# Kernel tuning notes

Hardware: AMD Instinct MI355X
Metric: run time of the kernel (lower is better)

Reference implementation:

```python
import jax, jax.numpy as jnp
import numpy as np
from jax import lax

B, N, C = 2, 4096, 8
MAX_DET = 100
SCORE_THR = 0.01
NMS_THR = 0.5
NEG = -1e30  # sentinel for masked scores


def setup_inputs() -> dict:
    key = jax.random.key(0)
    k1, k2, k3, k4, k5 = jax.random.split(key, 5)
    # valid xyxy boxes: centers in [0,512), extents in [2,66)
    ctr = jax.random.uniform(k1, (B, N, 2), dtype=jnp.float32) * 512.0
    wh = jax.random.uniform(k2, (B, N, 2), dtype=jnp.float32) * 64.0 + 2.0
    boxes = jnp.concatenate([ctr - wh / 2, ctr + wh / 2], axis=-1)  # [B,N,4]
    classification = jax.random.uniform(k3, (B, N, C), dtype=jnp.float32)
    rotation = jax.random.normal(k4, (B, N, 3), dtype=jnp.float32)
    translation = jax.random.normal(k5, (B, N, 3), dtype=jnp.float32)
    return {"boxes": boxes, "classification": classification,
            "rotation": rotation, "translation": translation}


def _pairwise_iou(b):
    # b: [N,4] xyxy, torchvision convention (no +1)
    x1, y1, x2, y2 = b[:, 0], b[:, 1], b[:, 2], b[:, 3]
    area = (x2 - x1) * (y2 - y1)
    ix1 = jnp.maximum(x1[:, None], x1[None, :])
    iy1 = jnp.maximum(y1[:, None], y1[None, :])
    ix2 = jnp.minimum(x2[:, None], x2[None, :])
    iy2 = jnp.minimum(y2[:, None], y2[None, :])
    inter = jnp.clip(ix2 - ix1, 0.0) * jnp.clip(iy2 - iy1, 0.0)
    union = area[:, None] + area[None, :] - inter
    return inter / jnp.maximum(union, 1e-9)


def _nms_keep(boxes, scores, valid):
    # greedy NMS matching torchvision.ops.nms on the `valid` subset.
    order = jnp.argsort(-jnp.where(valid, scores, NEG))  # score-descending
    iou = _pairwise_iou(boxes[order])  # [N,N]
    idx = jnp.arange(N)
    keep0 = valid[order]

    def body(i, keep):
        sup = keep[i] & (iou[i] > NMS_THR) & (idx > i)
        return keep & ~sup

    keep_sorted = lax.fori_loop(0, N, body, keep0)
    return jnp.zeros(N, bool).at[order].set(keep_sorted)


def _filter_image(boxes, cls, rot, trans):
    # boxes [N,4], cls [N,C], rot [N,3], trans [N,3]
    def per_class(scores):
        valid = scores > SCORE_THR
        keep = _nms_keep(boxes, scores, valid)
        return jnp.where(keep, scores, NEG)

    masked = jax.vmap(per_class, in_axes=1)(cls)  # [C,N]
    topv, topi = lax.top_k(masked.reshape(-1), MAX_DET)
    labels = topi // N
    anchors = topi % N
    ok = topv > NEG / 2
    okc = ok[:, None]
    boxes_o = jnp.where(okc, boxes[anchors], -1.0)
    scores_o = jnp.where(ok, topv, -1.0)
    labels_o = jnp.where(ok, labels, -1)
    rot_o = jnp.where(okc, rot[anchors], -1.0)
    trans_o = jnp.where(okc, trans[anchors], -1.0)
    return boxes_o, scores_o, labels_o, rot_o, trans_o


def reference(boxes, classification, rotation, translation):
    return jax.vmap(_filter_image)(boxes, classification, rotation, translation)
```

## Files before the change

kernel.cpp:

```cpp
#include <hip/hip_runtime.h>
#include <hip/hip_bf16.h>
#include <stdint.h>

#define B_ 2
#define N_ 4096
#define C_ 8
#define MAXDET 100
#define SCORE_THR 0.01f
#define NMS_THR 0.5f
#define NEGV -1e30f

typedef unsigned long long u64;

__device__ __forceinline__ unsigned mono_key(float f) {
    unsigned u = __float_as_uint(f);
    return (u & 0x80000000u) ? ~u : (u | 0x80000000u);
}
__device__ __forceinline__ float mono_dec(unsigned m) {
    return (m & 0x80000000u) ? __uint_as_float(m ^ 0x80000000u)
                             : __uint_as_float(~m);
}
__device__ __forceinline__ bool iou_gt_half(float inter, float uni) {
    return (inter + inter - uni) > uni * 0x1p-25f;
}
__device__ __forceinline__ void wave_fence() {
    asm volatile("s_waitcnt lgkmcnt(0)" ::: "memory");
}

__device__ __forceinline__ void ce_shfl(u64 &e0, u64 &e1, int tid, int size,
                                        int stride, bool desc) {
    const int m = stride >> 1;
    bool d = (((2 * tid) & size) == 0) ? desc : !desc;
    bool lower = (tid & m) == 0;
    u64 p0 = __shfl_xor(e0, m, 64);
    u64 p1 = __shfl_xor(e1, m, 64);
    bool takeMax = (d == lower);
    e0 = takeMax ? (e0 > p0 ? e0 : p0) : (e0 < p0 ? e0 : p0);
    e1 = takeMax ? (e1 > p1 ? e1 : p1) : (e1 < p1 ? e1 : p1);
}
__device__ __forceinline__ void ce_intra(u64 &e0, u64 &e1, int tid, int size,
                                         bool desc) {
    bool d = (((2 * tid) & size) == 0) ? desc : !desc;
    if ((e0 < e1) == d) { u64 t = e0; e0 = e1; e1 = t; }
}

__global__ __launch_bounds__(512) void sortA_kernel(
    const float* __restrict__ cls,
    u64* __restrict__ keys)
{
    __shared__ u64 k[1024];
    const int q = blockIdx.x;
    const int bc = blockIdx.y;
    const int b = bc >> 3, c = bc & 7;
    const int tid = threadIdx.x;
    const bool desc = ((q & 1) == 0);

    u64 e0, e1;
    {
        int i0 = q * 1024 + 2 * tid;
        float s0 = cls[((size_t)b * N_ + i0) * C_ + c];
        float s1 = cls[((size_t)b * N_ + i0 + 1) * C_ + c];
        float f0 = (s0 > SCORE_THR) ? s0 : NEGV;
        float f1 = (s1 > SCORE_THR) ? s1 : NEGV;
        e0 = ((u64)mono_key(f0) << 32) | (unsigned)(~i0);
        e1 = ((u64)mono_key(f1) << 32) | (unsigned)(~(i0 + 1));
    }

    #pragma unroll
    for (int size = 2; size <= 128; size <<= 1) {
        #pragma unroll
        for (int stride = size >> 1; stride >= 2; stride >>= 1)
            ce_shfl(e0, e1, tid, size, stride, desc);
        ce_intra(e0, e1, tid, size, desc);
    }
    #pragma unroll
    for (int size = 256; size <= 1024; size <<= 1) {
        k[2 * tid] = e0; k[2 * tid + 1] = e1;
        __syncthreads();
        for (int stride = size >> 1; stride >= 128; stride >>= 1) {
            int pos = 2 * tid - (tid & (stride - 1));
            int par = pos + stride;
            bool d = ((pos & size) == 0) ? desc : !desc;
            u64 a = k[pos], bb = k[par];
            if ((a < bb) == d) { k[pos] = bb; k[par] = a; }
            __syncthreads();
        }
        e0 = k[2 * tid]; e1 = k[2 * tid + 1];
        #pragma unroll
        for (int stride = 64; stride >= 2; stride >>= 1)
            ce_shfl(e0, e1, tid, size, stride, desc);
        ce_intra(e0, e1, tid, size, desc);
    }

    ulonglong2 v; v.x = e0; v.y = e1;
    *(ulonglong2*)&keys[(size_t)bc * N_ + q * 1024 + 2 * tid] = v;
}

__global__ __launch_bounds__(512) void fused_kernel(
    const u64* __restrict__ keys,
    const float* __restrict__ boxes,
    u64* __restrict__ cand)
{
    __shared__ u64 m[4096];
    __shared__ float4 sb192[192];
    __shared__ float  sa192[192];
    __shared__ u64 cm[576];
    __shared__ float4 sbx[64];
    __shared__ u64 shJ[64];
    __shared__ int s_fin;

    const int bc = blockIdx.x;
    const int b = bc >> 3, cls = bc & 7;
    const int tid = threadIdx.x;
    const int lane = tid & 63;
    const int wave = tid >> 6;
    const size_t kbase = (size_t)bc * N_;
    const float4* boxes4 = (const float4*)boxes;

    u64 e0, e1;
    {
        int i = 2 * tid;
        int qq = i >> 8;
        int off = qq * 1024 + ((qq & 1) ? 768 : 0) + (i & 255);
        ulonglong2 v = *(const ulonglong2*)&keys[kbase + off];
        e0 = v.x; e1 = v.y;
    }

    #pragma unroll
    for (int size = 512; size <= 1024; size <<= 1) {
        m[2 * tid] = e0; m[2 * tid + 1] = e1;
        __syncthreads();
        for (int stride = size >> 1; stride >= 128; stride >>= 1) {
            int pos = 2 * tid - (tid & (stride - 1));
            int par = pos + stride;
            bool d = ((pos & size) == 0);
            u64 a = m[pos], bb = m[par];
            if ((a < bb) == d) { m[pos] = bb; m[par] = a; }
            __syncthreads();
        }
        e0 = m[2 * tid]; e1 = m[2 * tid + 1];
        #pragma unroll
        for (int stride = 64; stride >= 2; stride >>= 1)
            ce_shfl(e0, e1, tid, size, stride, true);
        ce_intra(e0, e1, tid, size, true);
    }
    m[2 * tid] = e0; m[2 * tid + 1] = e1;
    __syncthreads();

    if (tid < 192) {
        int orig = (int)(~(unsigned)m[tid]);
        float4 bx = boxes4[(size_t)b * N_ + orig];
        sb192[tid] = bx;
        sa192[tid] = (bx.z - bx.x) * (bx.w - bx.y);
    }
    __syncthreads();

    for (int qq = tid; qq < 576; qq += 512) {
        int r = qq / 3, w = qq - 3 * r;
        int chunk = r >> 6;
        u64 bits = 0ull;
        if (w >= chunk) {
            float4 bi = sb192[r];
            float aarea = sa192[r];
            #pragma unroll 8
            for (int t = 0; t < 64; t++) {
                float4 bj = sb192[w * 64 + t];
                float barea = sa192[w * 64 + t];
                float ix1 = fmaxf(bi.x, bj.x);
                float iy1 = fmaxf(bi.y, bj.y);
                float ix2 = fminf(bi.z, bj.z);
                float iy2 = fminf(bi.w, bj.w);
                float inter = fmaxf(ix2 - ix1, 0.0f) * fmaxf(iy2 - iy1, 0.0f);
                float uni = fmaxf(aarea + barea - inter, 1e-9f);
                if (iou_gt_half(inter, uni)) bits |= (1ull << t);
            }
            if (w == chunk) bits &= ~((2ull << (r & 63)) - 1ull);
        }
        cm[qq] = bits;
    }
    __syncthreads();

    if (wave == 0) {
        u64 remv = 0ull;
        int cc = 0;
        bool fin = false;
        for (int c = 0; c < 3; c++) {
            int p = c * 64 + lane;
            u64 key = m[p];
            float sc = mono_dec((unsigned)(key >> 32));
            u64 validb = __ballot(sc > -1e29f);
            if (validb == 0ull) { fin = true; break; }

            u64 curw = __shfl(remv, c, 64);
            u64 kept = 0ull;
            for (int t = 0; t < 64; t++) {
                u64 iv = cm[(c * 64 + t) * 3 + c];
                u64 bit = 1ull << t;
                if (!(curw & bit) && (validb & bit)) { kept |= bit; curw |= iv; }
            }

            if ((kept >> lane) & 1ull) {
                int rank = cc + __popcll(kept & ((1ull << lane) - 1ull));
                if (rank < 128) {
                    int orig = (int)(~(unsigned)key);
                    unsigned flat = (unsigned)(cls * N_ + orig);
                    cand[bc * 128 + rank] =
                        ((u64)mono_key(sc) << 32) | (unsigned)(~flat);
                }
            }
            cc += __popcll(kept);
            if (cc >= 128) { fin = true; break; }

            if (lane < 3) {
                u64 acc = 0ull;
                for (int t = 0; t < 64; t++)
                    if ((kept >> t) & 1ull) acc |= cm[(c * 64 + t) * 3 + lane];
                remv |= acc;
            }
        }
        if (fin) {
            int filled = cc < 128 ? cc : 128;
            for (int s = lane; s < 128; s += 64)
                if (s >= filled) cand[bc * 128 + s] = 0ull;
        }
        if (lane == 0) s_fin = fin ? 1 : 0;
    }
    __syncthreads();
    if (s_fin) return;

    for (int i = tid; i < 4096; i += 512) m[i] = keys[kbase + i];
    __syncthreads();
    for (int size = 2048; size <= 4096; size <<= 1) {
        for (int stride = size >> 1; stride > 0; stride >>= 1) {
            for (int t = tid; t < 2048; t += 512) {
                int pos = 2 * t - (t & (stride - 1));
                int par = pos + stride;
                bool d = ((pos & size) == 0);
                u64 a = m[pos], bb = m[par];
                if ((a < bb) == d) { m[pos] = bb; m[par] = a; }
            }
            __syncthreads();
        }
    }
    if (wave != 0) return;

    {
        u64 remv = 0ull;
        int cc = 0;
        for (int c = 0; c < 64; c++) {
            int p = c * 64 + lane;
            u64 key = m[p];
            float sc = mono_dec((unsigned)(key >> 32));
            u64 validb = __ballot(sc > -1e29f);
            if (validb == 0ull) break;

            int orig = (int)(~(unsigned)key);
            float4 bl = boxes4[(size_t)b * N_ + orig];
            sbx[lane] = bl;
            wave_fence();
            float al = (bl.z - bl.x) * (bl.w - bl.y);

            u64 intra = 0ull;
            for (int t = 0; t < 64; t++) {
                float4 bj = sbx[t];
                float ab = (bj.z - bj.x) * (bj.w - bj.y);
                float ix1 = fmaxf(bl.x, bj.x);
                float iy1 = fmaxf(bl.y, bj.y);
                float ix2 = fminf(bl.z, bj.z);
                float iy2 = fminf(bl.w, bj.w);
                float inter = fmaxf(ix2 - ix1, 0.0f) * fmaxf(iy2 - iy1, 0.0f);
                float uni = fmaxf(al + ab - inter, 1e-9f);
                if (t > lane && iou_gt_half(inter, uni)) intra |= (1ull << t);
            }
            shJ[lane] = intra;
            wave_fence();

            u64 curw = __shfl(remv, c, 64);
            u64 kept = 0ull;
            for (int t = 0; t < 64; t++) {
                u64 iv = shJ[t];
                u64 bit = 1ull << t;
                if (!(curw & bit) && (validb & bit)) { kept |= bit; curw |= iv; }
            }

            if ((kept >> lane) & 1ull) {
                int rank = cc + __popcll(kept & ((1ull << lane) - 1ull));
                if (rank < 128) {
                    unsigned flat = (unsigned)(cls * N_ + orig);
                    cand[bc * 128 + rank] =
                        ((u64)mono_key(sc) << 32) | (unsigned)(~flat);
                }
            }
            cc += __popcll(kept);
            if (cc >= 128) break;

            if (lane > c) {
                u64 accw = 0ull;
                for (int u = 0; u < 64; u++) {
                    int pj = lane * 64 + u;
                    int oj = (int)(~(unsigned)m[pj]);
                    float4 bj = boxes4[(size_t)b * N_ + oj];
                    float ab = (bj.z - bj.x) * (bj.w - bj.y);
                    bool sup = false;
                    for (int tt = 0; tt < 64; tt++) {
                        if (!((kept >> tt) & 1ull)) continue;
                        float4 br = sbx[tt];
                        float ar = (br.z - br.x) * (br.w - br.y);
                        float ix1 = fmaxf(br.x, bj.x);
                        float iy1 = fmaxf(br.y, bj.y);
                        float ix2 = fminf(br.z, bj.z);
                        float iy2 = fminf(br.w, bj.w);
                        float inter = fmaxf(ix2 - ix1, 0.0f) * fmaxf(iy2 - iy1, 0.0f);
                        float uni = fmaxf(ar + ab - inter, 1e-9f);
                        if (iou_gt_half(inter, uni)) { sup = true; break; }
                    }
                    if (sup) accw |= (1ull << u);
                }
                remv |= accw;
            }
            wave_fence();
        }
        int filled = cc < 128 ? cc : 128;
        for (int s = lane; s < 128; s += 64)
            if (s >= filled) cand[bc * 128 + s] = 0ull;
    }
}

__global__ __launch_bounds__(1024) void merge_kernel(
    const u64* __restrict__ cand,
    const float* __restrict__ boxes,
    const float* __restrict__ rot,
    const float* __restrict__ trans,
    float* __restrict__ out)
{
    __shared__ u64 sk[1024];
    const int b = blockIdx.x;
    const int tid = threadIdx.x;
    const int c = tid >> 7, s = tid & 127;

    int src = (c & 1) ? (c * 128 + (127 - s)) : tid;
    sk[tid] = cand[(size_t)b * 1024 + src];

    for (int size = 256; size <= 1024; size <<= 1) {
        for (int stride = size >> 1; stride > 0; stride >>= 1) {
            __syncthreads();
            int partner = tid ^ stride;
            if (partner > tid) {
                bool desc = ((tid & size) == 0);
                u64 a = sk[tid], bb = sk[partner];
                if ((a < bb) == desc) { sk[tid] = bb; sk[partner] = a; }
            }
        }
    }
    __syncthreads();

    if (tid < MAXDET) {
        u64 key = sk[tid];
        float score = mono_dec((unsigned)(key >> 32));
        bool ok = score > (NEGV * 0.5f);
        unsigned flat = (~(unsigned)key) & 32767u;
        int cc = flat >> 12;
        int n = flat & (N_ - 1);

        float* obox = out;
        float* oscr = out + 800;
        float* olab = out + 1000;
        float* orot = out + 1200;
        float* otrn = out + 1800;

        #pragma unroll
        for (int d = 0; d < 4; d++)
            obox[b * 400 + tid * 4 + d] =
                ok ? boxes[((size_t)b * N_ + n) * 4 + d] : -1.0f;
        oscr[b * MAXDET + tid] = ok ? score : -1.0f;
        olab[b * MAXDET + tid] = ok ? (float)cc : -1.0f;
        #pragma unroll
        for (int d = 0; d < 3; d++) {
            orot[b * 300 + tid * 3 + d] =
                ok ? rot[((size_t)b * N_ + n) * 3 + d] : -1.0f;
            otrn[b * 300 + tid * 3 + d] =
                ok ? trans[((size_t)b * N_ + n) * 3 + d] : -1.0f;
        }
    }
}

extern "C" void kernel_launch(void* const* d_in, const int* in_sizes, int n_in,
                              void* d_out, int out_size, void* d_ws, size_t ws_size,
                              hipStream_t stream) {
    const float* boxes = (const float*)d_in[0];
    const float* cls   = (const float*)d_in[1];
    const float* rot   = (const float*)d_in[2];
    const float* trans = (const float*)d_in[3];
    float* out = (float*)d_out;

    char* w = (char*)d_ws;
    u64* keys = (u64*)w;   w += (size_t)B_ * C_ * N_ * sizeof(u64);
    u64* cand = (u64*)w;   w += (size_t)B_ * C_ * 128 * sizeof(u64);

    sortA_kernel<<<dim3(4, B_ * C_), 512, 0, stream>>>(cls, keys);
    fused_kernel<<<B_ * C_, 512, 0, stream>>>(keys, boxes, cand);
    merge_kernel<<<B_, 1024, 0, stream>>>(cand, boxes, rot, trans, out);
}
```

Before: 97.27 us.

## Fuse sort, NMS and merge into one kernel with last-block election

Replaces the three-kernel pipeline (per-quarter sort, per-class NMS, cross-class merge) with a single kernel. Each block sorts all four 1024-element quarters of its class in shared memory, and the last block to finish per image, chosen with an atomic counter, performs the final merge and output gather. This removes two kernel launches and the global round-trip of the key array. In exchange, each of the 16 blocks does the whole sort serially instead of spreading it over 64 blocks, and a memset is added to reset the counter.

```diff
diff --git a/kernel.cpp b/kernel.cpp
--- a/kernel.cpp
+++ b/kernel.cpp
@@ -1,5 +1,4 @@
 #include <hip/hip_runtime.h>
-#include <hip/hip_bf16.h>
 #include <stdint.h>
 
 #define B_ 2
@@ -43,29 +42,8 @@
     bool d = (((2 * tid) & size) == 0) ? desc : !desc;
     if ((e0 < e1) == d) { u64 t = e0; e0 = e1; e1 = t; }
 }
-
-__global__ __launch_bounds__(512) void sortA_kernel(
-    const float* __restrict__ cls,
-    u64* __restrict__ keys)
-{
-    __shared__ u64 k[1024];
-    const int q = blockIdx.x;
-    const int bc = blockIdx.y;
-    const int b = bc >> 3, c = bc & 7;
-    const int tid = threadIdx.x;
-    const bool desc = ((q & 1) == 0);
-
-    u64 e0, e1;
-    {
-        int i0 = q * 1024 + 2 * tid;
-        float s0 = cls[((size_t)b * N_ + i0) * C_ + c];
-        float s1 = cls[((size_t)b * N_ + i0 + 1) * C_ + c];
-        float f0 = (s0 > SCORE_THR) ? s0 : NEGV;
-        float f1 = (s1 > SCORE_THR) ? s1 : NEGV;
-        e0 = ((u64)mono_key(f0) << 32) | (unsigned)(~i0);
-        e1 = ((u64)mono_key(f1) << 32) | (unsigned)(~(i0 + 1));
-    }
-
+__device__ __forceinline__ void bitonic_reg128(u64 &e0, u64 &e1, int tid,
+                                               bool desc) {
     #pragma unroll
     for (int size = 2; size <= 128; size <<= 1) {
         #pragma unroll
@@ -73,82 +51,91 @@
             ce_shfl(e0, e1, tid, size, stride, desc);
         ce_intra(e0, e1, tid, size, desc);
     }
+}
+__device__ __forceinline__ void merge_hybrid(u64 &e0, u64 &e1, u64* k, int tid,
+                                             int size, bool desc) {
+    k[2 * tid] = e0; k[2 * tid + 1] = e1;
+    __syncthreads();
+    for (int stride = size >> 1; stride >= 128; stride >>= 1) {
+        int pos = 2 * tid - (tid & (stride - 1));
+        int par = pos + stride;
+        bool d = ((pos & size) == 0) ? desc : !desc;
+        u64 a = k[pos], bb = k[par];
+        if ((a < bb) == d) { k[pos] = bb; k[par] = a; }
+        __syncthreads();
+    }
+    e0 = k[2 * tid]; e1 = k[2 * tid + 1];
     #pragma unroll
-    for (int size = 256; size <= 1024; size <<= 1) {
-        k[2 * tid] = e0; k[2 * tid + 1] = e1;
-        __syncthreads();
-        for (int stride = size >> 1; stride >= 128; stride >>= 1) {
-            int pos = 2 * tid - (tid & (stride - 1));
-            int par = pos + stride;
-            bool d = ((pos & size) == 0) ? desc : !desc;
-            u64 a = k[pos], bb = k[par];
-            if ((a < bb) == d) { k[pos] = bb; k[par] = a; }
-            __syncthreads();
-        }
-        e0 = k[2 * tid]; e1 = k[2 * tid + 1];
-        #pragma unroll
-        for (int stride = 64; stride >= 2; stride >>= 1)
-            ce_shfl(e0, e1, tid, size, stride, desc);
-        ce_intra(e0, e1, tid, size, desc);
-    }
-
-    ulonglong2 v; v.x = e0; v.y = e1;
-    *(ulonglong2*)&keys[(size_t)bc * N_ + q * 1024 + 2 * tid] = v;
-}
-
-__global__ __launch_bounds__(512) void fused_kernel(
-    const u64* __restrict__ keys,
+    for (int stride = 64; stride >= 2; stride >>= 1)
+        ce_shfl(e0, e1, tid, size, stride, desc);
+    ce_intra(e0, e1, tid, size, desc);
+}
+
+__global__ __launch_bounds__(512) void mega_kernel(
+    const float* __restrict__ cls,
     const float* __restrict__ boxes,
-    u64* __restrict__ cand)
+    const float* __restrict__ rot,
+    const float* __restrict__ trans,
+    u64* __restrict__ cand,
+    int* __restrict__ cnt,
+    float* __restrict__ out)
 {
     __shared__ u64 m[4096];
+    __shared__ u64 scr[1024];
     __shared__ float4 sb192[192];
     __shared__ float  sa192[192];
     __shared__ u64 cm[576];
     __shared__ float4 sbx[64];
     __shared__ u64 shJ[64];
     __shared__ int s_fin;
+    __shared__ int s_elect;
 
     const int bc = blockIdx.x;
-    const int b = bc >> 3, cls = bc & 7;
+    const int b = bc >> 3, cls_id = bc & 7;
     const int tid = threadIdx.x;
     const int lane = tid & 63;
     const int wave = tid >> 6;
-    const size_t kbase = (size_t)bc * N_;
     const float4* boxes4 = (const float4*)boxes;
 
-    u64 e0, e1;
+    float sreg[8];
+    #pragma unroll
+    for (int q = 0; q < 4; q++) {
+        int i0 = q * 1024 + 2 * tid;
+        sreg[2 * q]     = cls[((size_t)b * N_ + i0) * C_ + cls_id];
+        sreg[2 * q + 1] = cls[((size_t)b * N_ + i0 + 1) * C_ + cls_id];
+    }
+
+    #pragma unroll 1
+    for (int q = 0; q < 4; q++) {
+        const bool desc = ((q & 1) == 0);
+        int i0 = q * 1024 + 2 * tid;
+        float f0 = (sreg[2 * q]     > SCORE_THR) ? sreg[2 * q]     : NEGV;
+        float f1 = (sreg[2 * q + 1] > SCORE_THR) ? sreg[2 * q + 1] : NEGV;
+        u64 e0 = ((u64)mono_key(f0) << 32) | (unsigned)(~i0);
+        u64 e1 = ((u64)mono_key(f1) << 32) | (unsigned)(~(i0 + 1));
+        u64* k = &m[q * 1024];
+        bitonic_reg128(e0, e1, tid, desc);
+        merge_hybrid(e0, e1, k, tid, 256, desc);
+        merge_hybrid(e0, e1, k, tid, 512, desc);
+        merge_hybrid(e0, e1, k, tid, 1024, desc);
+        k[2 * tid] = e0; k[2 * tid + 1] = e1;
+        __syncthreads();
+    }
+
     {
+        u64 e0, e1;
         int i = 2 * tid;
         int qq = i >> 8;
         int off = qq * 1024 + ((qq & 1) ? 768 : 0) + (i & 255);
-        ulonglong2 v = *(const ulonglong2*)&keys[kbase + off];
-        e0 = v.x; e1 = v.y;
-    }
-
-    #pragma unroll
-    for (int size = 512; size <= 1024; size <<= 1) {
-        m[2 * tid] = e0; m[2 * tid + 1] = e1;
-        __syncthreads();
-        for (int stride = size >> 1; stride >= 128; stride >>= 1) {
-            int pos = 2 * tid - (tid & (stride - 1));
-            int par = pos + stride;
-            bool d = ((pos & size) == 0);
-            u64 a = m[pos], bb = m[par];
-            if ((a < bb) == d) { m[pos] = bb; m[par] = a; }
-            __syncthreads();
-        }
-        e0 = m[2 * tid]; e1 = m[2 * tid + 1];
-        #pragma unroll
-        for (int stride = 64; stride >= 2; stride >>= 1)
-            ce_shfl(e0, e1, tid, size, stride, true);
-        ce_intra(e0, e1, tid, size, true);
-    }
-    m[2 * tid] = e0; m[2 * tid + 1] = e1;
+        e0 = m[off]; e1 = m[off + 1];
+        merge_hybrid(e0, e1, scr, tid, 512, true);
+        merge_hybrid(e0, e1, scr, tid, 1024, true);
+        scr[2 * tid] = e0; scr[2 * tid + 1] = e1;
+    }
     __syncthreads();
 
     if (tid < 192) {
-        int orig = (int)(~(unsigned)m[tid]);
+        int orig = (int)(~(unsigned)scr[tid]);
         float4 bx = boxes4[(size_t)b * N_ + orig];
         sb192[tid] = bx;
         sa192[tid] = (bx.z - bx.x) * (bx.w - bx.y);
@@ -186,7 +173,7 @@
         bool fin = false;
         for (int c = 0; c < 3; c++) {
             int p = c * 64 + lane;
-            u64 key = m[p];
+            u64 key = scr[p];
             float sc = mono_dec((unsigned)(key >> 32));
             u64 validb = __ballot(sc > -1e29f);
             if (validb == 0ull) { fin = true; break; }
@@ -203,7 +190,7 @@
                 int rank = cc + __popcll(kept & ((1ull << lane) - 1ull));
                 if (rank < 128) {
                     int orig = (int)(~(unsigned)key);
-                    unsigned flat = (unsigned)(cls * N_ + orig);
+                    unsigned flat = (unsigned)(cls_id * N_ + orig);
                     cand[bc * 128 + rank] =
                         ((u64)mono_key(sc) << 32) | (unsigned)(~flat);
                 }
@@ -226,160 +213,158 @@
         if (lane == 0) s_fin = fin ? 1 : 0;
     }
     __syncthreads();
-    if (s_fin) return;
-
-    for (int i = tid; i < 4096; i += 512) m[i] = keys[kbase + i];
-    __syncthreads();
-    for (int size = 2048; size <= 4096; size <<= 1) {
-        for (int stride = size >> 1; stride > 0; stride >>= 1) {
-            for (int t = tid; t < 2048; t += 512) {
-                int pos = 2 * t - (t & (stride - 1));
-                int par = pos + stride;
-                bool d = ((pos & size) == 0);
-                u64 a = m[pos], bb = m[par];
-                if ((a < bb) == d) { m[pos] = bb; m[par] = a; }
-            }
-            __syncthreads();
-        }
-    }
-    if (wave != 0) return;
+
+    if (!s_fin) {
+        for (int size = 2048; size <= 4096; size <<= 1) {
+            for (int stride = size >> 1; stride > 0; stride >>= 1) {
+                for (int t = tid; t < 2048; t += 512) {
+                    int pos = 2 * t - (t & (stride - 1));
+                    int par = pos + stride;
+                    bool d = ((pos & size) == 0);
+                    u64 a = m[pos], bb = m[par];
+                    if ((a < bb) == d) { m[pos] = bb; m[par] = a; }
+                }
+                __syncthreads();
+            }
+        }
+        if (wave == 0) {
+            u64 remv = 0ull;
+            int cc = 0;
+            for (int c = 0; c < 64; c++) {
+                int p = c * 64 + lane;
+                u64 key = m[p];
+                float sc = mono_dec((unsigned)(key >> 32));
+                u64 validb = __ballot(sc > -1e29f);
+                if (validb == 0ull) break;
+
+                int orig = (int)(~(unsigned)key);
+                float4 bl = boxes4[(size_t)b * N_ + orig];
+                sbx[lane] = bl;
+                wave_fence();
+                float al = (bl.z - bl.x) * (bl.w - bl.y);
+
+                u64 intra = 0ull;
+                for (int t = 0; t < 64; t++) {
+                    float4 bj = sbx[t];
+                    float ab = (bj.z - bj.x) * (bj.w - bj.y);
+                    float ix1 = fmaxf(bl.x, bj.x);
+                    float iy1 = fmaxf(bl.y, bj.y);
+                    float ix2 = fminf(bl.z, bj.z);
+                    float iy2 = fminf(bl.w, bj.w);
+                    float inter = fmaxf(ix2 - ix1, 0.0f) * fmaxf(iy2 - iy1, 0.0f);
+                    float uni = fmaxf(al + ab - inter, 1e-9f);
+                    if (t > lane && iou_gt_half(inter, uni)) intra |= (1ull << t);
+                }
+                shJ[lane] = intra;
+                wave_fence();
+
+                u64 curw = __shfl(remv, c, 64);
+                u64 kept = 0ull;
+                for (int t = 0; t < 64; t++) {
+                    u64 iv = shJ[t];
+                    u64 bit = 1ull << t;
+                    if (!(curw & bit) && (validb & bit)) { kept |= bit; curw |= iv; }
+                }
+
+                if ((kept >> lane) & 1ull) {
+                    int rank = cc + __popcll(kept & ((1ull << lane) - 1ull));
+                    if (rank < 128) {
+                        unsigned flat = (unsigned)(cls_id * N_ + orig);
+                        cand[bc * 128 + rank] =
+                            ((u64)mono_key(sc) << 32) | (unsigned)(~flat);
+                    }
+                }
+                cc += __popcll(kept);
+                if (cc >= 128) break;
+
+                if (lane > c) {
+                    u64 accw = 0ull;
+                    for (int u = 0; u < 64; u++) {
+                        int pj = lane * 64 + u;
+                        int oj = (int)(~(unsigned)m[pj]);
+                        float4 bj = boxes4[(size_t)b * N_ + oj];
+                        float ab = (bj.z - bj.x) * (bj.w - bj.y);
+                        bool sup = false;
+                        for (int tt = 0; tt < 64; tt++) {
+                            if (!((kept >> tt) & 1ull)) continue;
+                            float4 br = sbx[tt];
+                            float ar = (br.z - br.x) * (br.w - br.y);
+                            float ix1 = fmaxf(br.x, bj.x);
+                            float iy1 = fmaxf(br.y, bj.y);
+                            float ix2 = fminf(br.z, bj.z);
+                            float iy2 = fminf(br.w, bj.w);
+                            float inter = fmaxf(ix2 - ix1, 0.0f) * fmaxf(iy2 - iy1, 0.0f);
+                            float uni = fmaxf(ar + ab - inter, 1e-9f);
+                            if (iou_gt_half(inter, uni)) { sup = true; break; }
+                        }
+                        if (sup) accw |= (1ull << u);
+                    }
+                    remv |= accw;
+                }
+                wave_fence();
+            }
+            int filled = cc < 128 ? cc : 128;
+            for (int s = lane; s < 128; s += 64)
+                if (s >= filled) cand[bc * 128 + s] = 0ull;
+        }
+        __syncthreads();
+    }
+
+    __threadfence();
+    if (tid == 0) {
+        int old = atomicAdd(&cnt[b], 1);
+        s_elect = (old == 7) ? 1 : 0;
+    }
+    __syncthreads();
+    if (!s_elect) return;
+    __threadfence();
 
     {
-        u64 remv = 0ull;
-        int cc = 0;
-        for (int c = 0; c < 64; c++) {
-            int p = c * 64 + lane;
-            u64 key = m[p];
-            float sc = mono_dec((unsigned)(key >> 32));
-            u64 validb = __ballot(sc > -1e29f);
-            if (validb == 0ull) break;
-
-            int orig = (int)(~(unsigned)key);
-            float4 bl = boxes4[(size_t)b * N_ + orig];
-            sbx[lane] = bl;
-            wave_fence();
-            float al = (bl.z - bl.x) * (bl.w - bl.y);
-
-            u64 intra = 0ull;
-            for (int t = 0; t < 64; t++) {
-                float4 bj = sbx[t];
-                float ab = (bj.z - bj.x) * (bj.w - bj.y);
-                float ix1 = fmaxf(bl.x, bj.x);
-                float iy1 = fmaxf(bl.y, bj.y);
-                float ix2 = fminf(bl.z, bj.z);
-                float iy2 = fminf(bl.w, bj.w);
-                float inter = fmaxf(ix2 - ix1, 0.0f) * fmaxf(iy2 - iy1, 0.0f);
-                float uni = fmaxf(al + ab - inter, 1e-9f);
-                if (t > lane && iou_gt_half(inter, uni)) intra |= (1ull << t);
-            }
-            shJ[lane] = intra;
-            wave_fence();
-
-            u64 curw = __shfl(remv, c, 64);
-            u64 kept = 0ull;
-            for (int t = 0; t < 64; t++) {
-                u64 iv = shJ[t];
-                u64 bit = 1ull << t;
-                if (!(curw & bit) && (validb & bit)) { kept |= bit; curw |= iv; }
-            }
-
-            if ((kept >> lane) & 1ull) {
-                int rank = cc + __popcll(kept & ((1ull << lane) - 1ull));
-                if (rank < 128) {
-                    unsigned flat = (unsigned)(cls * N_ + orig);
-                    cand[bc * 128 + rank] =
-                        ((u64)mono_key(sc) << 32) | (unsigned)(~flat);
-                }
-            }
-            cc += __popcll(kept);
-            if (cc >= 128) break;
-
-            if (lane > c) {
-                u64 accw = 0ull;
-                for (int u = 0; u < 64; u++) {
-                    int pj = lane * 64 + u;
-                    int oj = (int)(~(unsigned)m[pj]);
-                    float4 bj = boxes4[(size_t)b * N_ + oj];
-                    float ab = (bj.z - bj.x) * (bj.w - bj.y);
-                    bool sup = false;
-                    for (int tt = 0; tt < 64; tt++) {
-                        if (!((kept >> tt) & 1ull)) continue;
-                        float4 br = sbx[tt];
-                        float ar = (br.z - br.x) * (br.w - br.y);
-                        float ix1 = fmaxf(br.x, bj.x);
-                        float iy1 = fmaxf(br.y, bj.y);
-                        float ix2 = fminf(br.z, bj.z);
-                        float iy2 = fminf(br.w, bj.w);
-                        float inter = fmaxf(ix2 - ix1, 0.0f) * fmaxf(iy2 - iy1, 0.0f);
-                        float uni = fmaxf(ar + ab - inter, 1e-9f);
-                        if (iou_gt_half(inter, uni)) { sup = true; break; }
-                    }
-                    if (sup) accw |= (1ull << u);
-                }
-                remv |= accw;
-            }
-            wave_fence();
-        }
-        int filled = cc < 128 ? cc : 128;
-        for (int s = lane; s < 128; s += 64)
-            if (s >= filled) cand[bc * 128 + s] = 0ull;
-    }
-}
-
-__global__ __launch_bounds__(1024) void merge_kernel(
-    const u64* __restrict__ cand,
-    const float* __restrict__ boxes,
-    const float* __restrict__ rot,
-    const float* __restrict__ trans,
-    float* __restrict__ out)
-{
-    __shared__ u64 sk[1024];
-    const int b = blockIdx.x;
-    const int tid = threadIdx.x;
-    const int c = tid >> 7, s = tid & 127;
-
-    int src = (c & 1) ? (c * 128 + (127 - s)) : tid;
-    sk[tid] = cand[(size_t)b * 1024 + src];
-
-    for (int size = 256; size <= 1024; size <<= 1) {
-        for (int stride = size >> 1; stride > 0; stride >>= 1) {
-            __syncthreads();
-            int partner = tid ^ stride;
-            if (partner > tid) {
-                bool desc = ((tid & size) == 0);
-                u64 a = sk[tid], bb = sk[partner];
-                if ((a < bb) == desc) { sk[tid] = bb; sk[partner] = a; }
-            }
-        }
-    }
-    __syncthreads();
-
-    if (tid < MAXDET) {
-        u64 key = sk[tid];
-        float score = mono_dec((unsigned)(key >> 32));
-        bool ok = score > (NEGV * 0.5f);
-        unsigned flat = (~(unsigned)key) & 32767u;
-        int cc = flat >> 12;
-        int n = flat & (N_ - 1);
-
-        float* obox = out;
-        float* oscr = out + 800;
-        float* olab = out + 1000;
-        float* orot = out + 1200;
-        float* otrn = out + 1800;
-
-        #pragma unroll
-        for (int d = 0; d < 4; d++)
-            obox[b * 400 + tid * 4 + d] =
-                ok ? boxes[((size_t)b * N_ + n) * 4 + d] : -1.0f;
-        oscr[b * MAXDET + tid] = ok ? score : -1.0f;
-        olab[b * MAXDET + tid] = ok ? (float)cc : -1.0f;
-        #pragma unroll
-        for (int d = 0; d < 3; d++) {
-            orot[b * 300 + tid * 3 + d] =
-                ok ? rot[((size_t)b * N_ + n) * 3 + d] : -1.0f;
-            otrn[b * 300 + tid * 3 + d] =
-                ok ? trans[((size_t)b * N_ + n) * 3 + d] : -1.0f;
+        const u64* candb = cand + (size_t)b * 1024;
+        int i = 2 * tid;
+        int c8 = i >> 7;
+        int ss = i & 127;
+        u64 f0, f1;
+        if (c8 & 1) {
+            f0 = candb[c8 * 128 + 127 - ss];
+            f1 = candb[c8 * 128 + 126 - ss];
+        } else {
+            f0 = candb[i];
+            f1 = candb[i + 1];
+        }
+        merge_hybrid(f0, f1, scr, tid, 256, true);
+        merge_hybrid(f0, f1, scr, tid, 512, true);
+        merge_hybrid(f0, f1, scr, tid, 1024, true);
+        scr[2 * tid] = f0; scr[2 * tid + 1] = f1;
+        __syncthreads();
+
+        if (tid < MAXDET) {
+            u64 key = scr[tid];
+            float score = mono_dec((unsigned)(key >> 32));
+            bool ok = score > (NEGV * 0.5f);
+            unsigned flat = (~(unsigned)key) & 32767u;
+            int cc8 = flat >> 12;
+            int n = flat & (N_ - 1);
+
+            float* obox = out;
+            float* oscr = out + 800;
+            float* olab = out + 1000;
+            float* orot = out + 1200;
+            float* otrn = out + 1800;
+
+            #pragma unroll
+            for (int d = 0; d < 4; d++)
+                obox[b * 400 + tid * 4 + d] =
+                    ok ? boxes[((size_t)b * N_ + n) * 4 + d] : -1.0f;
+            oscr[b * MAXDET + tid] = ok ? score : -1.0f;
+            olab[b * MAXDET + tid] = ok ? (float)cc8 : -1.0f;
+            #pragma unroll
+            for (int d = 0; d < 3; d++) {
+                orot[b * 300 + tid * 3 + d] =
+                    ok ? rot[((size_t)b * N_ + n) * 3 + d] : -1.0f;
+                otrn[b * 300 + tid * 3 + d] =
+                    ok ? trans[((size_t)b * N_ + n) * 3 + d] : -1.0f;
+            }
         }
     }
 }
@@ -394,10 +379,10 @@
     float* out = (float*)d_out;
 
     char* w = (char*)d_ws;
-    u64* keys = (u64*)w;   w += (size_t)B_ * C_ * N_ * sizeof(u64);
-    u64* cand = (u64*)w;   w += (size_t)B_ * C_ * 128 * sizeof(u64);
-
-    sortA_kernel<<<dim3(4, B_ * C_), 512, 0, stream>>>(cls, keys);
-    fused_kernel<<<B_ * C_, 512, 0, stream>>>(keys, boxes, cand);
-    merge_kernel<<<B_, 1024, 0, stream>>>(cand, boxes, rot, trans, out);
-}
+    u64* cand = (u64*)w;
+    int* cnt  = (int*)(w + 16384);
+
+    hipMemsetAsync(cnt, 0, 2 * sizeof(int), stream);
+    mega_kernel<<<B_ * C_, 512, 0, stream>>>(cls, boxes, rot, trans,
+                                             cand, cnt, out);
+}
```

After: 119.2 us. 22.5% more time.

## Fuse score sort into NMS kernel with register-resident full bitonic sort

Applied to the files above, without the earlier changes.

Removes the separate partial-sort kernel and keys workspace. Each of the 16 blocks now sorts all 4096 keys itself, holding 8 keys per thread in registers and using in-register and shuffle stages, with shared memory only for the large strides. The old fast path sorted only the top part of the list and needed a second full sort when NMS did not finish early. That fallback sort is gone because the full sort now happens up front. This saves a kernel launch and a global round trip, but each block does more sort work using only 16 blocks in total.

```diff
diff --git a/kernel.cpp b/kernel.cpp
--- a/kernel.cpp
+++ b/kernel.cpp
@@ -1,5 +1,4 @@
 #include <hip/hip_runtime.h>
-#include <hip/hip_bf16.h>
 #include <stdint.h>
 
 #define B_ 2
@@ -27,77 +26,8 @@
     asm volatile("s_waitcnt lgkmcnt(0)" ::: "memory");
 }
 
-__device__ __forceinline__ void ce_shfl(u64 &e0, u64 &e1, int tid, int size,
-                                        int stride, bool desc) {
-    const int m = stride >> 1;
-    bool d = (((2 * tid) & size) == 0) ? desc : !desc;
-    bool lower = (tid & m) == 0;
-    u64 p0 = __shfl_xor(e0, m, 64);
-    u64 p1 = __shfl_xor(e1, m, 64);
-    bool takeMax = (d == lower);
-    e0 = takeMax ? (e0 > p0 ? e0 : p0) : (e0 < p0 ? e0 : p0);
-    e1 = takeMax ? (e1 > p1 ? e1 : p1) : (e1 < p1 ? e1 : p1);
-}
-__device__ __forceinline__ void ce_intra(u64 &e0, u64 &e1, int tid, int size,
-                                         bool desc) {
-    bool d = (((2 * tid) & size) == 0) ? desc : !desc;
-    if ((e0 < e1) == d) { u64 t = e0; e0 = e1; e1 = t; }
-}
-
-__global__ __launch_bounds__(512) void sortA_kernel(
+__global__ __launch_bounds__(512) void sortnms_kernel(
     const float* __restrict__ cls,
-    u64* __restrict__ keys)
-{
-    __shared__ u64 k[1024];
-    const int q = blockIdx.x;
-    const int bc = blockIdx.y;
-    const int b = bc >> 3, c = bc & 7;
-    const int tid = threadIdx.x;
-    const bool desc = ((q & 1) == 0);
-
-    u64 e0, e1;
-    {
-        int i0 = q * 1024 + 2 * tid;
-        float s0 = cls[((size_t)b * N_ + i0) * C_ + c];
-        float s1 = cls[((size_t)b * N_ + i0 + 1) * C_ + c];
-        float f0 = (s0 > SCORE_THR) ? s0 : NEGV;
-        float f1 = (s1 > SCORE_THR) ? s1 : NEGV;
-        e0 = ((u64)mono_key(f0) << 32) | (unsigned)(~i0);
-        e1 = ((u64)mono_key(f1) << 32) | (unsigned)(~(i0 + 1));
-    }
-
-    #pragma unroll
-    for (int size = 2; size <= 128; size <<= 1) {
-        #pragma unroll
-        for (int stride = size >> 1; stride >= 2; stride >>= 1)
-            ce_shfl(e0, e1, tid, size, stride, desc);
-        ce_intra(e0, e1, tid, size, desc);
-    }
-    #pragma unroll
-    for (int size = 256; size <= 1024; size <<= 1) {
-        k[2 * tid] = e0; k[2 * tid + 1] = e1;
-        __syncthreads();
-        for (int stride = size >> 1; stride >= 128; stride >>= 1) {
-            int pos = 2 * tid - (tid & (stride - 1));
-            int par = pos + stride;
-            bool d = ((pos & size) == 0) ? desc : !desc;
-            u64 a = k[pos], bb = k[par];
-            if ((a < bb) == d) { k[pos] = bb; k[par] = a; }
-            __syncthreads();
-        }
-        e0 = k[2 * tid]; e1 = k[2 * tid + 1];
-        #pragma unroll
-        for (int stride = 64; stride >= 2; stride >>= 1)
-            ce_shfl(e0, e1, tid, size, stride, desc);
-        ce_intra(e0, e1, tid, size, desc);
-    }
-
-    ulonglong2 v; v.x = e0; v.y = e1;
-    *(ulonglong2*)&keys[(size_t)bc * N_ + q * 1024 + 2 * tid] = v;
-}
-
-__global__ __launch_bounds__(512) void fused_kernel(
-    const u64* __restrict__ keys,
     const float* __restrict__ boxes,
     u64* __restrict__ cand)
 {
@@ -110,41 +40,96 @@
     __shared__ int s_fin;
 
     const int bc = blockIdx.x;
-    const int b = bc >> 3, cls = bc & 7;
+    const int b = bc >> 3, cls_id = bc & 7;
     const int tid = threadIdx.x;
     const int lane = tid & 63;
     const int wave = tid >> 6;
-    const size_t kbase = (size_t)bc * N_;
     const float4* boxes4 = (const float4*)boxes;
 
-    u64 e0, e1;
-    {
-        int i = 2 * tid;
-        int qq = i >> 8;
-        int off = qq * 1024 + ((qq & 1) ? 768 : 0) + (i & 255);
-        ulonglong2 v = *(const ulonglong2*)&keys[kbase + off];
-        e0 = v.x; e1 = v.y;
-    }
-
+    u64 k[8];
     #pragma unroll
-    for (int size = 512; size <= 1024; size <<= 1) {
-        m[2 * tid] = e0; m[2 * tid + 1] = e1;
+    for (int j = 0; j < 8; j++) {
+        int i = tid * 8 + j;
+        float s = cls[((size_t)b * N_ + i) * C_ + cls_id];
+        float f = (s > SCORE_THR) ? s : NEGV;
+        k[j] = ((u64)mono_key(f) << 32) | (unsigned)(~i);
+    }
+
+    #pragma unroll
+    for (int size = 2; size <= 512; size <<= 1) {
+        #pragma unroll
+        for (int stride = size >> 1; stride >= 1; stride >>= 1) {
+            if (stride >= 8) {
+                const int ls = stride >> 3;
+                bool lower = ((tid & ls) == 0);
+                #pragma unroll
+                for (int j = 0; j < 8; j++) {
+                    int e = tid * 8 + j;
+                    bool d = ((e & size) == 0);
+                    u64 p = __shfl_xor(k[j], ls, 64);
+                    bool takeMax = (d == lower);
+                    k[j] = takeMax ? (k[j] > p ? k[j] : p)
+                                   : (k[j] < p ? k[j] : p);
+                }
+            } else {
+                #pragma unroll
+                for (int j = 0; j < 8; j++) {
+                    if ((j & stride) == 0) {
+                        int e = tid * 8 + j;
+                        bool d = ((e & size) == 0);
+                        u64 a = k[j], bb = k[j + stride];
+                        if ((a < bb) == d) { k[j] = bb; k[j + stride] = a; }
+                    }
+                }
+            }
+        }
+    }
+    #pragma unroll
+    for (int size = 1024; size <= 4096; size <<= 1) {
+        #pragma unroll
+        for (int j = 0; j < 8; j++) m[tid * 8 + j] = k[j];
         __syncthreads();
-        for (int stride = size >> 1; stride >= 128; stride >>= 1) {
-            int pos = 2 * tid - (tid & (stride - 1));
-            int par = pos + stride;
-            bool d = ((pos & size) == 0);
-            u64 a = m[pos], bb = m[par];
-            if ((a < bb) == d) { m[pos] = bb; m[par] = a; }
+        for (int stride = size >> 1; stride >= 512; stride >>= 1) {
+            for (int tt = tid; tt < 2048; tt += 512) {
+                int pos = 2 * tt - (tt & (stride - 1));
+                int par = pos + stride;
+                bool d = ((pos & size) == 0);
+                u64 a = m[pos], bb = m[par];
+                if ((a < bb) == d) { m[pos] = bb; m[par] = a; }
+            }
             __syncthreads();
         }
-        e0 = m[2 * tid]; e1 = m[2 * tid + 1];
-        #pragma unroll
-        for (int stride = 64; stride >= 2; stride >>= 1)
-            ce_shfl(e0, e1, tid, size, stride, true);
-        ce_intra(e0, e1, tid, size, true);
-    }
-    m[2 * tid] = e0; m[2 * tid + 1] = e1;
+        #pragma unroll
+        for (int j = 0; j < 8; j++) k[j] = m[tid * 8 + j];
+        #pragma unroll
+        for (int stride = 256; stride >= 1; stride >>= 1) {
+            if (stride >= 8) {
+                const int ls = stride >> 3;
+                bool lower = ((tid & ls) == 0);
+                #pragma unroll
+                for (int j = 0; j < 8; j++) {
+                    int e = tid * 8 + j;
+                    bool d = ((e & size) == 0);
+                    u64 p = __shfl_xor(k[j], ls, 64);
+                    bool takeMax = (d == lower);
+                    k[j] = takeMax ? (k[j] > p ? k[j] : p)
+                                   : (k[j] < p ? k[j] : p);
+                }
+            } else {
+                #pragma unroll
+                for (int j = 0; j < 8; j++) {
+                    if ((j & stride) == 0) {
+                        int e = tid * 8 + j;
+                        bool d = ((e & size) == 0);
+                        u64 a = k[j], bb = k[j + stride];
+                        if ((a < bb) == d) { k[j] = bb; k[j + stride] = a; }
+                    }
+                }
+            }
+        }
+    }
+    #pragma unroll
+    for (int j = 0; j < 8; j++) m[tid * 8 + j] = k[j];
     __syncthreads();
 
     if (tid < 192) {
@@ -203,7 +188,7 @@
                 int rank = cc + __popcll(kept & ((1ull << lane) - 1ull));
                 if (rank < 128) {
                     int orig = (int)(~(unsigned)key);
-                    unsigned flat = (unsigned)(cls * N_ + orig);
+                    unsigned flat = (unsigned)(cls_id * N_ + orig);
                     cand[bc * 128 + rank] =
                         ((u64)mono_key(sc) << 32) | (unsigned)(~flat);
                 }
@@ -228,22 +213,7 @@
     __syncthreads();
     if (s_fin) return;
 
-    for (int i = tid; i < 4096; i += 512) m[i] = keys[kbase + i];
-    __syncthreads();
-    for (int size = 2048; size <= 4096; size <<= 1) {
-        for (int stride = size >> 1; stride > 0; stride >>= 1) {
-            for (int t = tid; t < 2048; t += 512) {
-                int pos = 2 * t - (t & (stride - 1));
-                int par = pos + stride;
-                bool d = ((pos & size) == 0);
-                u64 a = m[pos], bb = m[par];
-                if ((a < bb) == d) { m[pos] = bb; m[par] = a; }
-            }
-            __syncthreads();
-        }
-    }
     if (wave != 0) return;
-
     {
         u64 remv = 0ull;
         int cc = 0;
@@ -286,7 +256,7 @@
             if ((kept >> lane) & 1ull) {
                 int rank = cc + __popcll(kept & ((1ull << lane) - 1ull));
                 if (rank < 128) {
-                    unsigned flat = (unsigned)(cls * N_ + orig);
+                    unsigned flat = (unsigned)(cls_id * N_ + orig);
                     cand[bc * 128 + rank] =
                         ((u64)mono_key(sc) << 32) | (unsigned)(~flat);
                 }
@@ -393,11 +363,8 @@
     const float* trans = (const float*)d_in[3];
     float* out = (float*)d_out;
 
-    char* w = (char*)d_ws;
-    u64* keys = (u64*)w;   w += (size_t)B_ * C_ * N_ * sizeof(u64);
-    u64* cand = (u64*)w;   w += (size_t)B_ * C_ * 128 * sizeof(u64);
-
-    sortA_kernel<<<dim3(4, B_ * C_), 512, 0, stream>>>(cls, keys);
-    fused_kernel<<<B_ * C_, 512, 0, stream>>>(keys, boxes, cand);
+    u64* cand = (u64*)d_ws;
+
+    sortnms_kernel<<<B_ * C_, 512, 0, stream>>>(cls, boxes, cand);
     merge_kernel<<<B_, 1024, 0, stream>>>(cand, boxes, rot, trans, out);
 }
```

New measurement: 112.3 us. 15.4% more time.
